# Kernel tuning notes

Measured on AMD Instinct MI355X. Metric: run time of the kernel, lower is better.

Reference implementation:

```python
import jax, jax.numpy as jnp
import numpy as np

V, E, H, T, B = 30000, 300, 300, 22, 4096

def setup_inputs() -> dict:
    key = jax.random.key(0)
    ks = jax.random.split(key, 10)
    cap = jax.random.randint(ks[0], (B, T), 0, V)
    cap_len = jax.random.randint(ks[1], (B,), 1, T + 1)  # valid lengths in [1, T]
    embed = jax.random.uniform(ks[2], (V, E), jnp.float32, -0.1, 0.1)
    s_ih = 1.0 / np.sqrt(H)
    W_ih = jax.random.uniform(ks[3], (4 * H, E), jnp.float32, -s_ih, s_ih)
    W_hh = jax.random.uniform(ks[4], (4 * H, H), jnp.float32, -s_ih, s_ih)
    b_ih = jax.random.uniform(ks[5], (4 * H,), jnp.float32, -s_ih, s_ih)
    b_hh = jax.random.uniform(ks[6], (4 * H,), jnp.float32, -s_ih, s_ih)
    v_wn = jax.random.normal(ks[7], (2, H), jnp.float32) * 0.05
    g_wn = jnp.linalg.norm(v_wn, axis=1)  # torch weight_norm init: g = ||v||
    b_cls = jnp.zeros((2,), jnp.float32)
    return {"cap": cap, "cap_len": cap_len, "embed": embed, "W_ih": W_ih,
            "W_hh": W_hh, "b_ih": b_ih, "b_hh": b_hh, "v_wn": v_wn,
            "g_wn": g_wn, "b_cls": b_cls}

def reference(cap, cap_len, embed, W_ih, W_hh, b_ih, b_hh, v_wn, g_wn, b_cls):
    Bn, Tn = cap.shape
    emb = embed[cap]                      # [B,T,E] embedding gather
    h0 = jnp.zeros((Bn, H), emb.dtype)
    c0 = jnp.zeros((Bn, H), emb.dtype)

    def step(carry, x_t):                 # x_t: [B,E]
        h, c = carry
        gates = x_t @ W_ih.T + b_ih + h @ W_hh.T + b_hh  # [B,4H]
        i, f, g, o = jnp.split(gates, 4, axis=-1)
        i = jax.nn.sigmoid(i); f = jax.nn.sigmoid(f); o = jax.nn.sigmoid(o)
        c = f * c + i * jnp.tanh(g)
        h = o * jnp.tanh(c)
        return (h, c), h

    _, hs = jax.lax.scan(step, (h0, c0), jnp.swapaxes(emb, 0, 1))  # hs: [T,B,H]
    hs = jnp.swapaxes(hs, 0, 1)                                    # [B,T,H]
    last = hs[jnp.arange(Bn), cap_len - 1]                         # [B,H] length-indexed gather
    # weight-normed linear head (dropout is identity at eval)
    W = g_wn[:, None] * v_wn / jnp.linalg.norm(v_wn, axis=1, keepdims=True)
    return last @ W.T + b_cls                                      # [B,2]
```

## Files before the change

kernel.cpp:

```cpp
#include <hip/hip_runtime.h>
#include <hip/hip_fp16.h>


#define TT 22
#define STEPS 22
#define NB 19
#define NWG 248
#define NTHR 1024
#define KTOT 20
#define BUFELT ((size_t)256 * KTOT * 512)
#define SROWS 27

typedef _Float16 f16;
typedef _Float16 f16x8 __attribute__((ext_vector_type(8)));
typedef float    f32x4 __attribute__((ext_vector_type(4)));

__device__ __forceinline__ float sigm(float x) { return 1.0f / (1.0f + __expf(-x)); }
__device__ __forceinline__ float tanh_f(float x) {
    float ax = fabsf(x);
    float e = __expf(-2.0f * ax);
    return copysignf((1.0f - e) / (1.0f + e), x);
}
__device__ __forceinline__ f16x8 pack8(float4 a, float4 b) {
    f16x8 v;
    v[0] = (f16)a.x; v[1] = (f16)a.y; v[2] = (f16)a.z; v[3] = (f16)a.w;
    v[4] = (f16)b.x; v[5] = (f16)b.y; v[6] = (f16)b.z; v[7] = (f16)b.w;
    return v;
}

__global__ __launch_bounds__(NTHR, 4)
void lstm_ws(const int* __restrict__ cap, const int* __restrict__ cap_len,
             const float* __restrict__ embed,
             const float* __restrict__ Wih, const float* __restrict__ Whh,
             const float* __restrict__ bih, const float* __restrict__ bhh,
             const float* __restrict__ v_wn, const float* __restrict__ g_wn,
             const float* __restrict__ b_cls,
             f16* __restrict__ bufs, int depth,
             unsigned* __restrict__ bar, float* __restrict__ out)
{
    __shared__ f16 Wl[80 * 512];
    __shared__ float ts[16][16][17];
    __shared__ int capS[SROWS][TT];
    __shared__ float scaleS[2];
    __shared__ int roleS;

    const int tid = threadIdx.x;
    const int wv = tid >> 6, ln = tid & 63, c = ln & 15, kg = ln >> 4;

    __builtin_amdgcn_fence(__ATOMIC_ACQUIRE, "agent");

    unsigned* cnt = bar + 12288;
    if (tid == 0) {
        unsigned xcc;
        asm volatile("s_getreg_b32 %0, hwreg(HW_REG_XCC_ID)" : "=s"(xcc));
        unsigned s = __hip_atomic_fetch_add(cnt + xcc * 64, 1u,
                                            __ATOMIC_RELAXED,
                                            __HIP_MEMORY_SCOPE_AGENT);
        roleS = (int)(xcc * 32 + s);
    }
    __syncthreads();
    const int grp = roleS >> 5;
    const int nb  = roleS & 31;
    if (nb >= NB) return;

    const int mrow0 = grp * 512;
    unsigned* flags = bar + grp * 1024;

    auto slot = [&](int n) { return bufs + (size_t)(n % depth) * BUFELT; };

    for (int u = tid; u < 80 * 64; u += NTHR) {
        int f = u >> 6, l = u & 63;
        int g = f / KTOT, kt = f - g * KTOT;
        int cc = l & 15, kgg = l >> 4;
        int jh0 = nb * 16 + cc;
        int j = g * 300 + jh0;
        int kb = kt * 32 + kgg * 8;
        f16x8 v;
        #pragma unroll
        for (int i = 0; i < 8; ++i) {
            int kk = kb + i;
            float x = 0.f;
            if (jh0 < 300) {
                if (kk < 300)                   x = Wih[(size_t)j * 300 + kk];
                else if (kk >= 320 && kk < 620) x = Whh[(size_t)j * 300 + (kk - 320)];
            }
            v[i] = (f16)x;
        }
        *(f16x8*)&Wl[(size_t)f * 512 + l * 8] = v;
    }

    const int srow0 = nb * SROWS;
    const int nr = (512 - srow0) < SROWS ? (512 - srow0) : SROWS;
    for (int u = tid; u < SROWS * TT; u += NTHR) {
        int rl = u / TT, t = u - rl * TT;
        if (rl < nr) capS[rl][t] = cap[(size_t)(mrow0 + srow0 + rl) * TT + t];
    }
    if (tid < 2) {
        float s = 0.f;
        for (int k = 0; k < 300; ++k) { float v = v_wn[tid * 300 + k]; s += v * v; }
        scaleS[tid] = g_wn[tid] * rsqrtf(s);
    }
    __syncthreads();

    auto stage_x = [&](int t, f16* bufn) {
        for (int u = tid; u < nr * 40; u += NTHR) {
            int rl = u / 40, k8 = u - rl * 40;
            int grow = mrow0 + srow0 + rl;
            const float* er = embed + (size_t)capS[rl][t] * 300;
            int k0 = k8 * 8;
            f16x8 v;
            if (k0 < 296) {
                v = pack8(*(const float4*)(er + k0), *(const float4*)(er + k0 + 4));
            } else if (k0 == 296) {
                float4 a = *(const float4*)(er + 296);
                v[0] = (f16)a.x; v[1] = (f16)a.y; v[2] = (f16)a.z; v[3] = (f16)a.w;
                v[4] = v[5] = v[6] = v[7] = (f16)0.f;
            } else {
                #pragma unroll
                for (int i = 0; i < 8; ++i) v[i] = (f16)0.f;
            }
            size_t off = ((size_t)((grow >> 4) * KTOT + (k8 >> 2))) * 512
                         + (grow & 15) * 32 + (k8 & 3) * 8;
            *(f16x8*)(bufn + off) = v;
        }
    };

    auto arrive = [&](unsigned ph) {
        __syncthreads();
        if (tid == 0)
            __hip_atomic_store(flags + nb * 32, ph, __ATOMIC_RELAXED,
                               __HIP_MEMORY_SCOPE_AGENT);
    };
    auto wait = [&](unsigned ph, bool fen) {
        if (tid < NB) {
            while (__hip_atomic_load(flags + tid * 32, __ATOMIC_RELAXED,
                                     __HIP_MEMORY_SCOPE_AGENT) < ph)
                __builtin_amdgcn_s_sleep(1);
        }
        if (fen)
            __builtin_amdgcn_fence(__ATOMIC_ACQUIRE, "agent");
        __syncthreads();
    };

    size_t aoff[2];
    #pragma unroll
    for (int m = 0; m < 2; ++m)
        aoff[m] = (size_t)(((mrow0 >> 4) + wv * 2 + m) * KTOT) * 512
                  + c * 32 + kg * 8;
    int wbase[4];
    #pragma unroll
    for (int g = 0; g < 4; ++g) wbase[g] = g * KTOT * 512 + ln * 8;

    const int jh = nb * 16 + c;
    float bias[4];
    #pragma unroll
    for (int g = 0; g < 4; ++g) {
        float bv = 0.f;
        if (jh < 300) { int j = g * 300 + jh; bv = bih[j] + bhh[j]; }
        bias[g] = bv;
    }
    int lenr[2][4];
    #pragma unroll
    for (int m = 0; m < 2; ++m) {
        int rb = mrow0 + wv * 32 + m * 16 + kg * 4;
        #pragma unroll
        for (int rg = 0; rg < 4; ++rg) lenr[m][rg] = cap_len[rb + rg];
    }
    const int hkt   = 10 + (nb >> 1);
    const int kbase = (nb & 1) * 16;

    float cst[2][4] = {};
    float hreg[2][4] = {};
    f32x4 acc[2][4];

    auto xpart = [&](const f16* bufc) {
        #pragma unroll
        for (int kt = 0; kt < 10; ++kt) {
            f16x8 av[2];
            #pragma unroll
            for (int m = 0; m < 2; ++m)
                av[m] = *(const f16x8*)(bufc + aoff[m] + kt * 512);
            #pragma unroll
            for (int g = 0; g < 4; ++g) {
                f16x8 bv = *(const f16x8*)&Wl[wbase[g] + kt * 512];
                #pragma unroll
                for (int m = 0; m < 2; ++m)
                    acc[m][g] = __builtin_amdgcn_mfma_f32_16x16x32_f16(av[m], bv, acc[m][g], 0, 0, 0);
            }
        }
    };
    auto hpart = [&](const f16* bufc) {
        #pragma unroll
        for (int kt = 10; kt < KTOT; ++kt) {
            f16x8 av[2];
            #pragma unroll
            for (int m = 0; m < 2; ++m)
                av[m] = *(const f16x8*)(bufc + aoff[m] + kt * 512);
            #pragma unroll
            for (int g = 0; g < 4; ++g) {
                f16x8 bv = *(const f16x8*)&Wl[wbase[g] + kt * 512];
                #pragma unroll
                for (int m = 0; m < 2; ++m)
                    acc[m][g] = __builtin_amdgcn_mfma_f32_16x16x32_f16(av[m], bv, acc[m][g], 0, 0, 0);
            }
        }
    };

    const bool ahead2 = (depth >= 3);
    stage_x(0, slot(0));
    if (ahead2) stage_x(1, slot(1));
    arrive(1);
    wait(1, false);

    #pragma unroll 1
    for (int t = 0; t < STEPS; ++t) {
        const f16* bufc = slot(t);
        #pragma unroll
        for (int m = 0; m < 2; ++m)
            #pragma unroll
            for (int g = 0; g < 4; ++g) {
                float bv = bias[g];
                f32x4 b4 = {bv, bv, bv, bv};
                acc[m][g] = b4;
            }

        bool reuse = (unsigned)(t + 1) >= (unsigned)depth;
        if (ahead2) {
            xpart(bufc);
            wait((unsigned)(t + 1), reuse);
        } else {
            wait((unsigned)(t + 1), reuse);
            xpart(bufc);
        }
        hpart(bufc);

        f16* bufn = slot(t + 1);
        #pragma unroll
        for (int m = 0; m < 2; ++m) {
            #pragma unroll
            for (int rg = 0; rg < 4; ++rg) {
                bool upd = (t < lenr[m][rg]);
                float iv = sigm(acc[m][0][rg]);
                float fv = sigm(acc[m][1][rg]);
                float gv = tanh_f(acc[m][2][rg]);
                float ov = sigm(acc[m][3][rg]);
                float cn = fv * cst[m][rg] + iv * gv;
                cn = upd ? cn : cst[m][rg];
                cst[m][rg] = cn;
                float hn = ov * tanh_f(cn);
                hreg[m][rg] = upd ? hn : hreg[m][rg];
                ts[wv][kg * 4 + rg][c] = (jh < 300) ? hreg[m][rg] : 0.f;
            }
            if (ln < 32) {
                int r = ln >> 1, hf = ln & 1;
                f16x8 v;
                #pragma unroll
                for (int i = 0; i < 8; ++i) v[i] = (f16)ts[wv][r][hf * 8 + i];
                int rtile = (mrow0 >> 4) + wv * 2 + m;
                size_t dst = ((size_t)(rtile * KTOT + hkt)) * 512
                             + r * 32 + kbase + hf * 8;
                *(f16x8*)(bufn + dst) = v;
            }
        }

        if (ahead2) { if (t + 2 < STEPS) stage_x(t + 2, slot(t + 2)); }
        else        { if (t + 1 < STEPS) stage_x(t + 1, slot(t + 1)); }
        arrive((unsigned)(t + 2));
    }

    wait((unsigned)(STEPS + 1), true);

    const f16* hb = slot(STEPS);
    for (int u = tid; u < nr * 2; u += NTHR) {
        int rl = u >> 1, cls = u & 1;
        int grow = mrow0 + srow0 + rl;
        float sc = scaleS[cls];
        const float* vr = v_wn + cls * 300;
        size_t rbase = ((size_t)((grow >> 4) * KTOT)) * 512 + (grow & 15) * 32;
        float s = 0.f;
        #pragma unroll 4
        for (int k = 0; k < 300; ++k) {
            int k2 = 320 + k;
            size_t off = rbase + (size_t)(k2 >> 5) * 512 + (k2 & 31);
            s += vr[k] * (float)hb[off];
        }
        out[(size_t)grow * 2 + cls] = sc * s + b_cls[cls];
    }
}

extern "C" void kernel_launch(void* const* d_in, const int* in_sizes, int n_in,
                              void* d_out, int out_size, void* d_ws, size_t ws_size,
                              hipStream_t stream) {
    const int*   cap     = (const int*)  d_in[0];
    const int*   cap_len = (const int*)  d_in[1];
    const float* embed   = (const float*)d_in[2];
    const float* W_ih    = (const float*)d_in[3];
    const float* W_hh    = (const float*)d_in[4];
    const float* b_ih    = (const float*)d_in[5];
    const float* b_hh    = (const float*)d_in[6];
    const float* v_wn    = (const float*)d_in[7];
    const float* g_wn    = (const float*)d_in[8];
    const float* b_cls   = (const float*)d_in[9];
    float* out = (float*)d_out;

    unsigned* bar = (unsigned*)d_ws;
    f16* bufs = (f16*)((char*)d_ws + 65536);
    size_t slot_bytes = BUFELT * sizeof(f16);
    int depth = (int)((ws_size > 65536 ? ws_size - 65536 : 0) / slot_bytes);
    if (depth > STEPS + 1) depth = STEPS + 1;
    if (depth < 2) depth = 2;

    hipMemsetAsync(bar, 0, 65536, stream);
    hipMemsetAsync(bufs, 0, slot_bytes, stream);

    lstm_ws<<<NWG, NTHR, 0, stream>>>(cap, cap_len, embed, W_ih, W_hh, b_ih, b_hh,
                                      v_wn, g_wn, b_cls, bufs, depth, bar, out);
}
```

Measured before the change: 422.9 us.

## Write h directly to global as scalars, drop LDS transpose, cap buffer depth

Removes the shared-memory transpose tile for the new hidden state; each lane now stores its f16 h values straight into the global staging buffer with scalar 2-byte writes. Embedding gathers switch to nontemporal loads, the W tile in LDS is enlarged, and the ring-buffer depth is capped at 3. The intent is to cut LDS traffic and a sync-free transpose step per timestep and to keep the staging ring small and cache-resident. The cost is many narrow uncoalesced global stores per step, and a shallow ring that may force more buffer-reuse waits.

Result: slower. 660.9 us (+56.3%).

```diff
diff --git a/kernel.cpp b/kernel.cpp
--- a/kernel.cpp
+++ b/kernel.cpp
@@ -14,6 +14,7 @@
 typedef _Float16 f16;
 typedef _Float16 f16x8 __attribute__((ext_vector_type(8)));
 typedef float    f32x4 __attribute__((ext_vector_type(4)));
+typedef float    fv4   __attribute__((ext_vector_type(4)));
 
 __device__ __forceinline__ float sigm(float x) { return 1.0f / (1.0f + __expf(-x)); }
 __device__ __forceinline__ float tanh_f(float x) {
@@ -21,7 +22,7 @@
     float e = __expf(-2.0f * ax);
     return copysignf((1.0f - e) / (1.0f + e), x);
 }
-__device__ __forceinline__ f16x8 pack8(float4 a, float4 b) {
+__device__ __forceinline__ f16x8 pack8v(fv4 a, fv4 b) {
     f16x8 v;
     v[0] = (f16)a.x; v[1] = (f16)a.y; v[2] = (f16)a.z; v[3] = (f16)a.w;
     v[4] = (f16)b.x; v[5] = (f16)b.y; v[6] = (f16)b.z; v[7] = (f16)b.w;
@@ -38,8 +39,7 @@
              f16* __restrict__ bufs, int depth,
              unsigned* __restrict__ bar, float* __restrict__ out)
 {
-    __shared__ f16 Wl[80 * 512];
-    __shared__ float ts[16][16][17];
+    __shared__ f16 Wl[84 * 512];
     __shared__ int capS[SROWS][TT];
     __shared__ float scaleS[2];
     __shared__ int roleS;
@@ -110,9 +110,11 @@
             int k0 = k8 * 8;
             f16x8 v;
             if (k0 < 296) {
-                v = pack8(*(const float4*)(er + k0), *(const float4*)(er + k0 + 4));
+                fv4 a = __builtin_nontemporal_load((const fv4*)(er + k0));
+                fv4 bb = __builtin_nontemporal_load((const fv4*)(er + k0 + 4));
+                v = pack8v(a, bb);
             } else if (k0 == 296) {
-                float4 a = *(const float4*)(er + 296);
+                fv4 a = __builtin_nontemporal_load((const fv4*)(er + 296));
                 v[0] = (f16)a.x; v[1] = (f16)a.y; v[2] = (f16)a.z; v[3] = (f16)a.w;
                 v[4] = v[5] = v[6] = v[7] = (f16)0.f;
             } else {
@@ -166,8 +168,9 @@
         #pragma unroll
         for (int rg = 0; rg < 4; ++rg) lenr[m][rg] = cap_len[rb + rg];
     }
-    const int hkt   = 10 + (nb >> 1);
-    const int kbase = (nb & 1) * 16;
+    const int hkt  = (320 + jh) >> 5;
+    const int hkgd = ((320 + jh) >> 3) & 3;
+    const int hel  = jh & 7;
 
     float cst[2][4] = {};
     float hreg[2][4] = {};
@@ -237,6 +240,8 @@
         f16* bufn = slot(t + 1);
         #pragma unroll
         for (int m = 0; m < 2; ++m) {
+            int rtile = (mrow0 >> 4) + wv * 2 + m;
+            size_t hb = ((size_t)(rtile * KTOT + hkt)) * 512 + hkgd * 8 + hel;
             #pragma unroll
             for (int rg = 0; rg < 4; ++rg) {
                 bool upd = (t < lenr[m][rg]);
@@ -249,17 +254,8 @@
                 cst[m][rg] = cn;
                 float hn = ov * tanh_f(cn);
                 hreg[m][rg] = upd ? hn : hreg[m][rg];
-                ts[wv][kg * 4 + rg][c] = (jh < 300) ? hreg[m][rg] : 0.f;
-            }
-            if (ln < 32) {
-                int r = ln >> 1, hf = ln & 1;
-                f16x8 v;
-                #pragma unroll
-                for (int i = 0; i < 8; ++i) v[i] = (f16)ts[wv][r][hf * 8 + i];
-                int rtile = (mrow0 >> 4) + wv * 2 + m;
-                size_t dst = ((size_t)(rtile * KTOT + hkt)) * 512
-                             + r * 32 + kbase + hf * 8;
-                *(f16x8*)(bufn + dst) = v;
+                f16 hv = (jh < 300) ? (f16)hreg[m][rg] : (f16)0.f;
+                bufn[hb + (size_t)(kg * 4 + rg) * 32] = hv;
             }
         }
 
@@ -281,7 +277,7 @@
         #pragma unroll 4
         for (int k = 0; k < 300; ++k) {
             int k2 = 320 + k;
-            size_t off = rbase + (size_t)(k2 >> 5) * 512 + (k2 & 31);
+            size_t off = rbase + (size_t)(k2 >> 5) * 512 + ((k2 >> 3) & 3) * 8 + (k2 & 7);
             s += vr[k] * (float)hb[off];
         }
         out[(size_t)grow * 2 + cls] = sc * s + b_cls[cls];
@@ -307,7 +303,7 @@
     f16* bufs = (f16*)((char*)d_ws + 65536);
     size_t slot_bytes = BUFELT * sizeof(f16);
     int depth = (int)((ws_size > 65536 ? ws_size - 65536 : 0) / slot_bytes);
-    if (depth > STEPS + 1) depth = STEPS + 1;
+    if (depth > 3) depth = 3;
     if (depth < 2) depth = 2;
 
     hipMemsetAsync(bar, 0, 65536, stream);
```
